# Optimization experiments

Hardware: AMD Instinct MI355X
Metric: run time of the kernel (lower is better)

Reference implementation:

```python
import jax, jax.numpy as jnp
import numpy as np

DMODEL = 1024
HEADS = 16
HEAD_SIZE = DMODEL // HEADS


def setup_inputs() -> dict:
    key = jax.random.key(0)
    ks = jax.random.split(key, 9)
    s = 1.0 / np.sqrt(DMODEL)
    x = jax.random.normal(ks[0], (4, 2048, DMODEL), dtype=jnp.float32)
    Wq = jax.random.uniform(ks[1], (DMODEL, DMODEL), jnp.float32, -s, s)
    bq = jax.random.uniform(ks[2], (DMODEL,), jnp.float32, -s, s)
    Wk = jax.random.uniform(ks[3], (DMODEL, DMODEL), jnp.float32, -s, s)
    bk = jax.random.uniform(ks[4], (DMODEL,), jnp.float32, -s, s)
    Wv = jax.random.uniform(ks[5], (DMODEL, DMODEL), jnp.float32, -s, s)
    bv = jax.random.uniform(ks[6], (DMODEL,), jnp.float32, -s, s)
    Wo = jax.random.uniform(ks[7], (DMODEL, DMODEL), jnp.float32, -s, s)
    bo = jax.random.uniform(ks[8], (DMODEL,), jnp.float32, -s, s)
    return {"x": x, "Wq": Wq, "bq": bq, "Wk": Wk, "bk": bk,
            "Wv": Wv, "bv": bv, "Wo": Wo, "bo": bo}


def _split_heads(t):
    b, s, _ = t.shape
    return t.reshape(b, s, HEADS, HEAD_SIZE).transpose(0, 2, 1, 3)  # [b,h,s,d]


def reference(x, Wq, bq, Wk, bk, Wv, bv, Wo, bo):
    q = _split_heads(x @ Wq.T + bq)
    k = _split_heads(x @ Wk.T + bk)
    v = _split_heads(x @ Wv.T + bv)
    scale = 1.0 / jnp.sqrt(jnp.float32(HEAD_SIZE))
    scores = jnp.einsum("bhqd,bhkd->bhqk", q, k) * scale  # full [B,H,S,S]
    attn = jax.nn.softmax(scores, axis=-1)
    out = jnp.einsum("bhqk,bhkd->bhqd", attn, v)
    b, h, s, d = out.shape
    out = out.transpose(0, 2, 1, 3).reshape(b, s, h * d)
    return out @ Wo.T + bo
```

## Files before the change

kernel.cpp:

```cpp
#include <hip/hip_runtime.h>

typedef _Float16 f16x8 __attribute__((ext_vector_type(8)));
typedef _Float16 f16x4 __attribute__((ext_vector_type(4)));
typedef float f32x4 __attribute__((ext_vector_type(4)));

#define MFMA16(a, b, c) __builtin_amdgcn_mfma_f32_16x16x32_f16(a, b, c, 0, 0, 0)

static constexpr int DM   = 1024;
static constexpr int SEQ  = 2048;
static constexpr int NHEAD = 16;
static constexpr int HD   = 64;

__device__ __forceinline__ void gload16(const _Float16* g, _Float16* l) {
  __builtin_amdgcn_global_load_lds((const __attribute__((address_space(1))) void*)g,
                                   (__attribute__((address_space(3))) void*)l, 16, 0, 0);
}

__device__ __forceinline__ float fexp2(float x) {
  float y; asm("v_exp_f32 %0, %1" : "=v"(y) : "v"(x)); return y;
}

__global__ __launch_bounds__(256) void cvt_kernel(
    const float* __restrict__ x,  const float* __restrict__ wq,
    const float* __restrict__ wk, const float* __restrict__ wv,
    const float* __restrict__ wo, _Float16* __restrict__ dst)
{
  const int NX4 = 2097152;
  const int NW4 = 262144;
  const int total = NX4 + 4 * NW4;
  for (int i = blockIdx.x * blockDim.x + threadIdx.x; i < total;
       i += gridDim.x * blockDim.x) {
    const float* src; size_t doff; int off;
    if (i < NX4) { src = x; off = i; doff = (size_t)i * 4; }
    else {
      int j = i - NX4; int wi = j >> 18; off = j & (NW4 - 1);
      src = wi == 0 ? wq : wi == 1 ? wk : wi == 2 ? wv : wo;
      doff = 8388608u + (size_t)wi * 1048576u + (size_t)off * 4;
    }
    f32x4 v = *(const f32x4*)(src + (size_t)off * 4);
    f16x4 hh;
    hh[0] = (_Float16)v[0]; hh[1] = (_Float16)v[1];
    hh[2] = (_Float16)v[2]; hh[3] = (_Float16)v[3];
    *(f16x4*)(dst + doff) = hh;
  }
}

__device__ __forceinline__ void gemm_core(
    const _Float16* __restrict__ Abase, const _Float16* __restrict__ Bbase,
    int K, _Float16* As, _Float16* Bs, int w, int l, int wr, int wc,
    f32x4 acc[4][4])
{
  const int l15 = l & 15, lg = l >> 4;
  const int r4 = l >> 2, kq = (l & 3) * 8;
  const int rowA0 = w * 16 + r4, rowA1 = 64 + w * 16 + r4;
  const int nsteps = K / 32;

  #define STAGE_G(k0, buf)                                                             \
    do {                                                                               \
      gload16(Abase + (size_t)rowA0 * K + (k0) + kq, As + (buf) * 4096 + w * 512 + l * 8);        \
      gload16(Abase + (size_t)rowA1 * K + (k0) + kq, As + (buf) * 4096 + 2048 + w * 512 + l * 8); \
      gload16(Bbase + (size_t)rowA0 * K + (k0) + kq, Bs + (buf) * 4096 + w * 512 + l * 8);        \
      gload16(Bbase + (size_t)rowA1 * K + (k0) + kq, Bs + (buf) * 4096 + 2048 + w * 512 + l * 8); \
    } while (0)

  STAGE_G(0, 0);
  STAGE_G(32, 1);
  asm volatile("s_waitcnt vmcnt(4)" ::: "memory");

  int cur = 0, pre = 2;
  for (int t = 0; t < nsteps; t++) {
    __builtin_amdgcn_s_barrier();
    asm volatile("" ::: "memory");

    if (t + 2 < nsteps) STAGE_G((t + 2) * 32, pre);

    const _Float16* as = As + cur * 4096;
    const _Float16* bs = Bs + cur * 4096;
    f16x8 af[4], bfr[4];
    #pragma unroll
    for (int mt = 0; mt < 4; mt++)
      af[mt] = *(const f16x8*)(as + (wr * 64 + mt * 16 + l15) * 32 + lg * 8);
    #pragma unroll
    for (int nt = 0; nt < 4; nt++)
      bfr[nt] = *(const f16x8*)(bs + (wc * 64 + nt * 16 + l15) * 32 + lg * 8);

    __builtin_amdgcn_s_setprio(1);
    #pragma unroll
    for (int mt = 0; mt < 4; mt++)
      #pragma unroll
      for (int nt = 0; nt < 4; nt++)
        acc[mt][nt] = MFMA16(af[mt], bfr[nt], acc[mt][nt]);
    __builtin_amdgcn_s_setprio(0);

    if (t < nsteps - 1) {
      asm volatile("s_waitcnt lgkmcnt(0)" ::: "memory");
      if (t + 2 < nsteps) asm volatile("s_waitcnt vmcnt(4)" ::: "memory");
      else                asm volatile("s_waitcnt vmcnt(0)" ::: "memory");
      __builtin_amdgcn_sched_barrier(0);
    }
    cur = cur == 2 ? 0 : cur + 1;
    pre = pre == 2 ? 0 : pre + 1;
  }
  #undef STAGE_G
}

__global__ __launch_bounds__(256) void qkv_gemm(
    const _Float16* __restrict__ xh,
    const _Float16* __restrict__ wqh, const _Float16* __restrict__ wkh,
    const _Float16* __restrict__ wvh,
    const float* __restrict__ bq, const float* __restrict__ bk,
    const float* __restrict__ bv,
    _Float16* __restrict__ qo, _Float16* __restrict__ ko,
    _Float16* __restrict__ vto)
{
  __shared__ __attribute__((aligned(16))) _Float16 As[12288], Bs[12288];
  const int tid = threadIdx.x, w = tid >> 6, l = tid & 63;
  const int l15 = l & 15, lg = l >> 4;
  const int wr = w >> 1, wc = w & 1;
  const int bx = blockIdx.x;
  const int sel = bx >> 3;
  const int n0 = (bx & 7) * 128;
  const int m0 = blockIdx.y * 128;
  const _Float16* W = sel == 0 ? wqh : sel == 1 ? wkh : wvh;
  const float* bias = sel == 0 ? bq : sel == 1 ? bk : bv;

  f32x4 acc[4][4] = {};
  gemm_core(xh + (size_t)m0 * DM, W + (size_t)n0 * DM, DM, As, Bs, w, l, wr, wc, acc);

  float biasv[4];
  #pragma unroll
  for (int nt = 0; nt < 4; nt++) biasv[nt] = bias[n0 + wc * 64 + nt * 16 + l15];

  if (sel < 2) {
    _Float16* outp = sel == 0 ? qo : ko;
    #pragma unroll
    for (int mt = 0; mt < 4; mt++) {
      int row = m0 + wr * 64 + mt * 16 + lg * 4;
      #pragma unroll
      for (int nt = 0; nt < 4; nt++) {
        int col = n0 + wc * 64 + nt * 16 + l15;
        #pragma unroll
        for (int r = 0; r < 4; r++)
          outp[(size_t)(row + r) * DM + col] = (_Float16)(acc[mt][nt][r] + biasv[nt]);
      }
    }
  } else {
    #pragma unroll
    for (int mt = 0; mt < 4; mt++) {
      int row0 = m0 + wr * 64 + mt * 16 + lg * 4;
      int b = row0 >> 11, s0 = row0 & 2047;
      #pragma unroll
      for (int nt = 0; nt < 4; nt++) {
        int col = n0 + wc * 64 + nt * 16 + l15;
        int hh = col >> 6, d = col & 63;
        f16x4 pk;
        #pragma unroll
        for (int r = 0; r < 4; r++) pk[r] = (_Float16)(acc[mt][nt][r] + biasv[nt]);
        *(f16x4*)(vto + ((size_t)((b * NHEAD + hh) * HD + d)) * SEQ + s0) = pk;
      }
    }
  }
}

__global__ __launch_bounds__(512, 3) void attn_kernel(
    const _Float16* __restrict__ qh, const _Float16* __restrict__ kh,
    const _Float16* __restrict__ vth, _Float16* __restrict__ atth)
{
  __shared__ __attribute__((aligned(16))) _Float16 Ks[3][4096];
  __shared__ __attribute__((aligned(16))) _Float16 Vs[3][4096];

  const int gid = blockIdx.x;
  const int bh = gid & 63, qt = gid >> 6;
  const int b = bh >> 4, h = bh & 15;
  const int tid = threadIdx.x, w = tid >> 6, l = tid & 63;
  const int l15 = l & 15, lg = l >> 4;
  const int q0 = qt * 256 + w * 32;

  const float c2 = 0.125f * 1.4426950408889634f;
  const _Float16 hc2 = (_Float16)c2;

  const _Float16* qbase = qh + (size_t)(b * SEQ + q0) * DM + h * HD;
  f16x8 aq[2][2];
  #pragma unroll
  for (int g = 0; g < 2; g++)
    #pragma unroll
    for (int ks = 0; ks < 2; ks++) {
      f16x8 v = *(const f16x8*)(qbase + (size_t)(g * 16 + l15) * DM + ks * 32 + lg * 8);
      #pragma unroll
      for (int j = 0; j < 8; j++) v[j] *= hc2;
      aq[g][ks] = v;
    }

  const _Float16* kbase = kh + (size_t)b * SEQ * DM + h * HD;
  const _Float16* vbase = vth + (size_t)bh * HD * SEQ;

  const int s0 = tid;
  const int kr0 = s0 >> 3, kc0 = (s0 & 7) ^ (kr0 & 7);

  f32x4 o[2][4] = {};
  f32x4 lr[2] = {};
  f16x8 ones;
  #pragma unroll
  for (int j = 0; j < 8; j++) ones[j] = (_Float16)1.0f;

  #pragma unroll
  for (int t0 = 0; t0 < 2; t0++) {
    const int kv = t0 * 64;
    gload16(kbase + (size_t)(kv + kr0) * DM + kc0 * 8, &Ks[t0][s0 * 8]);
    gload16(vbase + (size_t)kr0 * SEQ + kv + kc0 * 8, &Vs[t0][s0 * 8]);
  }
  asm volatile("s_waitcnt vmcnt(2)" ::: "memory");

  int cur = 0, pre = 2;
  for (int t = 0; t < 32; t++) {
    __builtin_amdgcn_s_barrier();
    asm volatile("" ::: "memory");

    if (t < 30) {
      const int kv2 = (t + 2) * 64;
      gload16(kbase + (size_t)(kv2 + kr0) * DM + kc0 * 8, &Ks[pre][s0 * 8]);
      gload16(vbase + (size_t)kr0 * SEQ + kv2 + kc0 * 8, &Vs[pre][s0 * 8]);
    }

    const _Float16* kb = &Ks[cur][0];
    const _Float16* vb = &Vs[cur][0];
    f16x8 bkf[4][2], vf[4][2];
    #pragma unroll
    for (int nt = 0; nt < 4; nt++)
      #pragma unroll
      for (int ks = 0; ks < 2; ks++) {
        const int off = (nt * 16 + l15) * 64 + (((ks * 4 + lg) ^ (l15 & 7)) << 3);
        bkf[nt][ks] = *(const f16x8*)&kb[off];
        vf[nt][ks]  = *(const f16x8*)&vb[off];
      }

    #pragma unroll
    for (int g = 0; g < 2; g++) {
      f32x4 sc[4] = {};
      __builtin_amdgcn_s_setprio(1);
      #pragma unroll
      for (int nt = 0; nt < 4; nt++) {
        sc[nt] = MFMA16(bkf[nt][0], aq[g][0], sc[nt]);
        sc[nt] = MFMA16(bkf[nt][1], aq[g][1], sc[nt]);
      }
      __builtin_amdgcn_s_setprio(0);

      unsigned pkA[4], pkB[4];
      #pragma unroll
      for (int nt = 0; nt < 4; nt++) {
        float e0 = fexp2(sc[nt][0]), e1 = fexp2(sc[nt][1]);
        float e2 = fexp2(sc[nt][2]), e3 = fexp2(sc[nt][3]);
        pkA[nt] = __builtin_bit_cast(unsigned, __builtin_amdgcn_cvt_pkrtz(e0, e1));
        pkB[nt] = __builtin_bit_cast(unsigned, __builtin_amdgcn_cvt_pkrtz(e2, e3));
      }
      f16x8 pa[2];
      #pragma unroll
      for (int ks = 0; ks < 2; ks++) {
        unsigned a0 = pkA[2 * ks], a1 = pkA[2 * ks + 1];
        unsigned b0 = pkB[2 * ks], b1 = pkB[2 * ks + 1];
        asm("v_permlane32_swap_b32 %0, %1" : "+v"(a0), "+v"(a1));
        asm("v_permlane16_swap_b32 %0, %1" : "+v"(a0), "+v"(a1));
        asm("v_permlane32_swap_b32 %0, %1" : "+v"(b0), "+v"(b1));
        asm("v_permlane16_swap_b32 %0, %1" : "+v"(b0), "+v"(b1));
        union { unsigned u[4]; f16x8 v; } pk;
        pk.u[0] = a0; pk.u[1] = b0; pk.u[2] = a1; pk.u[3] = b1;
        pa[ks] = pk.v;
      }
      __builtin_amdgcn_s_setprio(1);
      lr[g] = MFMA16(pa[0], ones, lr[g]);
      lr[g] = MFMA16(pa[1], ones, lr[g]);
      #pragma unroll
      for (int nt = 0; nt < 4; nt++) {
        o[g][nt] = MFMA16(pa[0], vf[nt][0], o[g][nt]);
        o[g][nt] = MFMA16(pa[1], vf[nt][1], o[g][nt]);
      }
      __builtin_amdgcn_s_setprio(0);
    }

    if (t < 31) {
      asm volatile("s_waitcnt lgkmcnt(0)" ::: "memory");
      if (t < 30) asm volatile("s_waitcnt vmcnt(2)" ::: "memory");
      else        asm volatile("s_waitcnt vmcnt(0)" ::: "memory");
      __builtin_amdgcn_sched_barrier(0);
    }
    cur = cur == 2 ? 0 : cur + 1;
    pre = pre == 2 ? 0 : pre + 1;
  }

  #pragma unroll
  for (int g = 0; g < 2; g++)
    #pragma unroll
    for (int r = 0; r < 4; r++) {
      float inv = 1.f / lr[g][r];
      int row = q0 + g * 16 + lg * 4 + r;
      #pragma unroll
      for (int nt = 0; nt < 4; nt++)
        atth[(size_t)(b * SEQ + row) * DM + h * HD + nt * 16 + l15] =
            (_Float16)(o[g][nt][r] * inv);
    }
}

__global__ __launch_bounds__(256) void out_gemm(
    const _Float16* __restrict__ ah, const _Float16* __restrict__ woh,
    const float* __restrict__ bo, float* __restrict__ out)
{
  __shared__ __attribute__((aligned(16))) _Float16 As[12288], Bs[12288];
  const int tid = threadIdx.x, w = tid >> 6, l = tid & 63;
  const int l15 = l & 15, lg = l >> 4;
  const int wr = w >> 1, wc = w & 1;
  const int n0 = blockIdx.x * 128;
  const int m0 = blockIdx.y * 128;

  f32x4 acc[4][4] = {};
  gemm_core(ah + (size_t)m0 * DM, woh + (size_t)n0 * DM, DM, As, Bs, w, l, wr, wc, acc);

  float biasv[4];
  #pragma unroll
  for (int nt = 0; nt < 4; nt++) biasv[nt] = bo[n0 + wc * 64 + nt * 16 + l15];
  #pragma unroll
  for (int mt = 0; mt < 4; mt++) {
    int row = m0 + wr * 64 + mt * 16 + lg * 4;
    #pragma unroll
    for (int nt = 0; nt < 4; nt++) {
      int col = n0 + wc * 64 + nt * 16 + l15;
      #pragma unroll
      for (int r = 0; r < 4; r++)
        out[(size_t)(row + r) * DM + col] = acc[mt][nt][r] + biasv[nt];
    }
  }
}

extern "C" void kernel_launch(void* const* d_in, const int* in_sizes, int n_in,
                              void* d_out, int out_size, void* d_ws, size_t ws_size,
                              hipStream_t stream)
{
  const float* x  = (const float*)d_in[0];
  const float* Wq = (const float*)d_in[1];
  const float* bq = (const float*)d_in[2];
  const float* Wk = (const float*)d_in[3];
  const float* bk = (const float*)d_in[4];
  const float* Wv = (const float*)d_in[5];
  const float* bv = (const float*)d_in[6];
  const float* Wo = (const float*)d_in[7];
  const float* bo = (const float*)d_in[8];
  float* out = (float*)d_out;

  _Float16* base = (_Float16*)d_ws;
  _Float16* xh  = base;
  _Float16* wqh = base + 8388608;
  _Float16* wkh = base + 9437184;
  _Float16* wvh = base + 10485760;
  _Float16* woh = base + 11534336;
  _Float16* qhp = base + 12582912;
  _Float16* khp = base + 20971520;
  _Float16* vth = base + 29360128;
  _Float16* ath = xh;

  cvt_kernel<<<1024, 256, 0, stream>>>(x, Wq, Wk, Wv, Wo, base);
  qkv_gemm<<<dim3(24, 64), 256, 0, stream>>>(xh, wqh, wkh, wvh, bq, bk, bv, qhp, khp, vth);
  attn_kernel<<<512, 512, 0, stream>>>(qhp, khp, vth, ath);
  out_gemm<<<dim3(8, 64), 256, 0, stream>>>(ath, woh, bo, out);
}
```

Baseline: 204.9 us.

## Switch to double-buffered pipelines and smaller attention blocks for occupancy

The GEMM core and the attention loop move from triple to double buffering, with prefetch distance one and a full vmcnt(0) wait each iteration. Shared memory per block drops, and launch bounds now ask for three blocks per CU. The attention kernel is split into 256-thread blocks covering 128 queries, with twice as many blocks. Inside the attention loop, the V fragment loads are deferred until after the softmax for both row groups, and the PV MFMAs are grouped together. The aim is higher occupancy to hide latency, at the cost of less in-flight prefetch per block and more redundant K/V loading across blocks.

```diff
diff --git a/kernel.cpp b/kernel.cpp
--- a/kernel.cpp
+++ b/kernel.cpp
@@ -64,15 +64,14 @@
     } while (0)
 
   STAGE_G(0, 0);
-  STAGE_G(32, 1);
-  asm volatile("s_waitcnt vmcnt(4)" ::: "memory");
-
-  int cur = 0, pre = 2;
+  asm volatile("s_waitcnt vmcnt(0)" ::: "memory");
+
+  int cur = 0;
   for (int t = 0; t < nsteps; t++) {
     __builtin_amdgcn_s_barrier();
     asm volatile("" ::: "memory");
 
-    if (t + 2 < nsteps) STAGE_G((t + 2) * 32, pre);
+    if (t + 1 < nsteps) STAGE_G((t + 1) * 32, cur ^ 1);
 
     const _Float16* as = As + cur * 4096;
     const _Float16* bs = Bs + cur * 4096;
@@ -92,19 +91,17 @@
         acc[mt][nt] = MFMA16(af[mt], bfr[nt], acc[mt][nt]);
     __builtin_amdgcn_s_setprio(0);
 
-    if (t < nsteps - 1) {
+    if (t + 1 < nsteps) {
       asm volatile("s_waitcnt lgkmcnt(0)" ::: "memory");
-      if (t + 2 < nsteps) asm volatile("s_waitcnt vmcnt(4)" ::: "memory");
-      else                asm volatile("s_waitcnt vmcnt(0)" ::: "memory");
+      asm volatile("s_waitcnt vmcnt(0)" ::: "memory");
       __builtin_amdgcn_sched_barrier(0);
     }
-    cur = cur == 2 ? 0 : cur + 1;
-    pre = pre == 2 ? 0 : pre + 1;
+    cur ^= 1;
   }
   #undef STAGE_G
 }
 
-__global__ __launch_bounds__(256) void qkv_gemm(
+__global__ __launch_bounds__(256, 3) void qkv_gemm(
     const _Float16* __restrict__ xh,
     const _Float16* __restrict__ wqh, const _Float16* __restrict__ wkh,
     const _Float16* __restrict__ wvh,
@@ -113,7 +110,7 @@
     _Float16* __restrict__ qo, _Float16* __restrict__ ko,
     _Float16* __restrict__ vto)
 {
-  __shared__ __attribute__((aligned(16))) _Float16 As[12288], Bs[12288];
+  __shared__ __attribute__((aligned(16))) _Float16 As[8192], Bs[8192];
   const int tid = threadIdx.x, w = tid >> 6, l = tid & 63;
   const int l15 = l & 15, lg = l >> 4;
   const int wr = w >> 1, wc = w & 1;
@@ -162,19 +159,19 @@
   }
 }
 
-__global__ __launch_bounds__(512, 3) void attn_kernel(
+__global__ __launch_bounds__(256, 3) void attn_kernel(
     const _Float16* __restrict__ qh, const _Float16* __restrict__ kh,
     const _Float16* __restrict__ vth, _Float16* __restrict__ atth)
 {
-  __shared__ __attribute__((aligned(16))) _Float16 Ks[3][4096];
-  __shared__ __attribute__((aligned(16))) _Float16 Vs[3][4096];
+  __shared__ __attribute__((aligned(16))) _Float16 Ks[2][4096];
+  __shared__ __attribute__((aligned(16))) _Float16 Vs[2][4096];
 
   const int gid = blockIdx.x;
   const int bh = gid & 63, qt = gid >> 6;
   const int b = bh >> 4, h = bh & 15;
   const int tid = threadIdx.x, w = tid >> 6, l = tid & 63;
   const int l15 = l & 15, lg = l >> 4;
-  const int q0 = qt * 256 + w * 32;
+  const int q0 = qt * 128 + w * 32;
 
   const float c2 = 0.125f * 1.4426950408889634f;
   const _Float16 hc2 = (_Float16)c2;
@@ -194,8 +191,17 @@
   const _Float16* kbase = kh + (size_t)b * SEQ * DM + h * HD;
   const _Float16* vbase = vth + (size_t)bh * HD * SEQ;
 
-  const int s0 = tid;
+  const int s0 = w * 64 + l, s1 = 256 + s0;
   const int kr0 = s0 >> 3, kc0 = (s0 & 7) ^ (kr0 & 7);
+  const int kr1 = s1 >> 3, kc1 = (s1 & 7) ^ (kr1 & 7);
+
+  #define STAGE_A(kv, buf)                                                        \
+    do {                                                                          \
+      gload16(kbase + (size_t)((kv) + kr0) * DM + kc0 * 8, &Ks[buf][s0 * 8]);     \
+      gload16(kbase + (size_t)((kv) + kr1) * DM + kc1 * 8, &Ks[buf][s1 * 8]);     \
+      gload16(vbase + (size_t)kr0 * SEQ + (kv) + kc0 * 8, &Vs[buf][s0 * 8]);      \
+      gload16(vbase + (size_t)kr1 * SEQ + (kv) + kc1 * 8, &Vs[buf][s1 * 8]);      \
+    } while (0)
 
   f32x4 o[2][4] = {};
   f32x4 lr[2] = {};
@@ -203,37 +209,25 @@
   #pragma unroll
   for (int j = 0; j < 8; j++) ones[j] = (_Float16)1.0f;
 
-  #pragma unroll
-  for (int t0 = 0; t0 < 2; t0++) {
-    const int kv = t0 * 64;
-    gload16(kbase + (size_t)(kv + kr0) * DM + kc0 * 8, &Ks[t0][s0 * 8]);
-    gload16(vbase + (size_t)kr0 * SEQ + kv + kc0 * 8, &Vs[t0][s0 * 8]);
-  }
-  asm volatile("s_waitcnt vmcnt(2)" ::: "memory");
-
-  int cur = 0, pre = 2;
+  STAGE_A(0, 0);
+  asm volatile("s_waitcnt vmcnt(0)" ::: "memory");
+
+  int cur = 0;
   for (int t = 0; t < 32; t++) {
     __builtin_amdgcn_s_barrier();
     asm volatile("" ::: "memory");
 
-    if (t < 30) {
-      const int kv2 = (t + 2) * 64;
-      gload16(kbase + (size_t)(kv2 + kr0) * DM + kc0 * 8, &Ks[pre][s0 * 8]);
-      gload16(vbase + (size_t)kr0 * SEQ + kv2 + kc0 * 8, &Vs[pre][s0 * 8]);
-    }
+    if (t < 31) STAGE_A((t + 1) * 64, cur ^ 1);
 
     const _Float16* kb = &Ks[cur][0];
-    const _Float16* vb = &Vs[cur][0];
-    f16x8 bkf[4][2], vf[4][2];
+    f16x8 bkf[4][2];
     #pragma unroll
     for (int nt = 0; nt < 4; nt++)
       #pragma unroll
-      for (int ks = 0; ks < 2; ks++) {
-        const int off = (nt * 16 + l15) * 64 + (((ks * 4 + lg) ^ (l15 & 7)) << 3);
-        bkf[nt][ks] = *(const f16x8*)&kb[off];
-        vf[nt][ks]  = *(const f16x8*)&vb[off];
-      }
-
+      for (int ks = 0; ks < 2; ks++)
+        bkf[nt][ks] = *(const f16x8*)&kb[(nt * 16 + l15) * 64 + (((ks * 4 + lg) ^ (l15 & 7)) << 3)];
+
+    f16x8 pa[2][2];
     #pragma unroll
     for (int g = 0; g < 2; g++) {
       f32x4 sc[4] = {};
@@ -253,7 +247,6 @@
         pkA[nt] = __builtin_bit_cast(unsigned, __builtin_amdgcn_cvt_pkrtz(e0, e1));
         pkB[nt] = __builtin_bit_cast(unsigned, __builtin_amdgcn_cvt_pkrtz(e2, e3));
       }
-      f16x8 pa[2];
       #pragma unroll
       for (int ks = 0; ks < 2; ks++) {
         unsigned a0 = pkA[2 * ks], a1 = pkA[2 * ks + 1];
@@ -264,28 +257,39 @@
         asm("v_permlane16_swap_b32 %0, %1" : "+v"(b0), "+v"(b1));
         union { unsigned u[4]; f16x8 v; } pk;
         pk.u[0] = a0; pk.u[1] = b0; pk.u[2] = a1; pk.u[3] = b1;
-        pa[ks] = pk.v;
-      }
-      __builtin_amdgcn_s_setprio(1);
-      lr[g] = MFMA16(pa[0], ones, lr[g]);
-      lr[g] = MFMA16(pa[1], ones, lr[g]);
-      #pragma unroll
-      for (int nt = 0; nt < 4; nt++) {
-        o[g][nt] = MFMA16(pa[0], vf[nt][0], o[g][nt]);
-        o[g][nt] = MFMA16(pa[1], vf[nt][1], o[g][nt]);
-      }
-      __builtin_amdgcn_s_setprio(0);
-    }
+        pa[g][ks] = pk.v;
+      }
+    }
+
+    const _Float16* vb = &Vs[cur][0];
+    f16x8 vf[4][2];
+    #pragma unroll
+    for (int nt = 0; nt < 4; nt++)
+      #pragma unroll
+      for (int ks = 0; ks < 2; ks++)
+        vf[nt][ks] = *(const f16x8*)&vb[(nt * 16 + l15) * 64 + (((ks * 4 + lg) ^ (l15 & 7)) << 3)];
+
+    __builtin_amdgcn_s_setprio(1);
+    #pragma unroll
+    for (int g = 0; g < 2; g++) {
+      lr[g] = MFMA16(pa[g][0], ones, lr[g]);
+      lr[g] = MFMA16(pa[g][1], ones, lr[g]);
+      #pragma unroll
+      for (int nt = 0; nt < 4; nt++) {
+        o[g][nt] = MFMA16(pa[g][0], vf[nt][0], o[g][nt]);
+        o[g][nt] = MFMA16(pa[g][1], vf[nt][1], o[g][nt]);
+      }
+    }
+    __builtin_amdgcn_s_setprio(0);
 
     if (t < 31) {
       asm volatile("s_waitcnt lgkmcnt(0)" ::: "memory");
-      if (t < 30) asm volatile("s_waitcnt vmcnt(2)" ::: "memory");
-      else        asm volatile("s_waitcnt vmcnt(0)" ::: "memory");
+      asm volatile("s_waitcnt vmcnt(0)" ::: "memory");
       __builtin_amdgcn_sched_barrier(0);
     }
-    cur = cur == 2 ? 0 : cur + 1;
-    pre = pre == 2 ? 0 : pre + 1;
-  }
+    cur ^= 1;
+  }
+  #undef STAGE_A
 
   #pragma unroll
   for (int g = 0; g < 2; g++)
@@ -300,11 +304,11 @@
     }
 }
 
-__global__ __launch_bounds__(256) void out_gemm(
+__global__ __launch_bounds__(256, 3) void out_gemm(
     const _Float16* __restrict__ ah, const _Float16* __restrict__ woh,
     const float* __restrict__ bo, float* __restrict__ out)
 {
-  __shared__ __attribute__((aligned(16))) _Float16 As[12288], Bs[12288];
+  __shared__ __attribute__((aligned(16))) _Float16 As[8192], Bs[8192];
   const int tid = threadIdx.x, w = tid >> 6, l = tid & 63;
   const int l15 = l & 15, lg = l >> 4;
   const int wr = w >> 1, wc = w & 1;
@@ -358,6 +362,6 @@
 
   cvt_kernel<<<1024, 256, 0, stream>>>(x, Wq, Wk, Wv, Wo, base);
   qkv_gemm<<<dim3(24, 64), 256, 0, stream>>>(xh, wqh, wkh, wvh, bq, bk, bv, qhp, khp, vth);
-  attn_kernel<<<512, 512, 0, stream>>>(qhp, khp, vth, ath);
+  attn_kernel<<<1024, 256, 0, stream>>>(qhp, khp, vth, ath);
   out_gemm<<<dim3(8, 64), 256, 0, stream>>>(ath, woh, bo, out);
 }
```

After: 181.9 us. -11.2%, faster.
